# Optimization experiments

Hardware: AMD Instinct MI355X
Metric: run time of the kernel (lower is better)

## Reference

```python
import jax, jax.numpy as jnp
import numpy as np
from jax import lax

B, C, N, T, K = 16, 64, 512, 64, 3
EPS = 1e-5


def _bn(x, g, b):
    # training-mode BatchNorm2d over (B, H=N, W=T) per channel
    m = jnp.mean(x, axis=(0, 2, 3), keepdims=True)
    v = jnp.var(x, axis=(0, 2, 3), keepdims=True)
    return (x - m) * lax.rsqrt(v + EPS) * g[None, :, None, None] + b[None, :, None, None]


def _conv(x, w, b, pad):
    y = lax.conv_general_dilated(x, w, (1, 1), ((0, 0), pad),
                                 dimension_numbers=('NCHW', 'OIHW', 'NCHW'))
    return y + b[None, :, None, None]


def setup_inputs() -> dict:
    key = jax.random.key(0)
    ks = jax.random.split(key, 8)
    xav = lambda k, sh, fi, fo: jax.random.normal(k, sh, jnp.float32) * np.sqrt(2.0 / (fi + fo))
    return {
        'x': jax.random.normal(ks[0], (B, C, N, T), jnp.float32),
        'adj_mx': jax.random.normal(ks[1], (K, N, N), jnp.float32) / np.sqrt(N),
        'cheb_w': xav(ks[2], (K, C, C), C, C),
        'cheb_b': jnp.zeros((C,), jnp.float32),
        'w1': xav(ks[3], (C, C, 1, 3), 3 * C, 3 * C),
        'b1': jnp.zeros((C,), jnp.float32),
        'g1': jnp.ones((C,), jnp.float32),
        'be1': jnp.zeros((C,), jnp.float32),
        'w2': xav(ks[4], (C, C, 1, 3), 3 * C, 3 * C),
        'b2': jnp.zeros((C,), jnp.float32),
        'g2': jnp.ones((C,), jnp.float32),
        'be2': jnp.zeros((C,), jnp.float32),
        'gate_w': xav(ks[5], (C, 2 * C, 1, 1), 2 * C, C),
        'gate_b': jnp.zeros((C,), jnp.float32),
        'res_w': xav(ks[6], (C, C, 1, 1), C, C),
        'res_b': jnp.zeros((C,), jnp.float32),
        'g3': jnp.ones((C,), jnp.float32),
        'be3': jnp.zeros((C,), jnp.float32),
    }


def _forward(x, adj_mx, cheb_w, cheb_b, w1, b1, g1, be1, w2, b2, g2, be2,
             gate_w, gate_b, res_w, res_b, g3, be3):
    # ChebFilterBlock: out[b,o,n,t] = sum_{k,i,m} x[b,i,m,t] adj[k,m,n] W[k,i,o] + bias
    spatial = jnp.einsum('bimt,kmn,kio->bont', x, adj_mx, cheb_w) \
              + cheb_b[None, :, None, None]
    # temporal branch: two (1,3) convs with BN+ReLU
    t = jax.nn.relu(_bn(_conv(x, w1, b1, (1, 1)), g1, be1))
    t = jax.nn.relu(_bn(_conv(t, w2, b2, (1, 1)), g2, be2))
    # gated fusion
    comb = jnp.concatenate([spatial, t], axis=1)
    gate = jax.nn.sigmoid(_conv(comb, gate_w, gate_b, (0, 0)))
    res = _conv(x, res_w, res_b, (0, 0))
    out = gate * spatial + (1.0 - gate) * t + res
    return _bn(out, g3, be3)


def reference(x, adj_mx, cheb_w, cheb_b, w1, b1, g1, be1, w2, b2, g2, be2,
              gate_w, gate_b, res_w, res_b, g3, be3):
    return _forward(x, adj_mx, cheb_w, cheb_b, w1, b1, g1, be1, w2, b2, g2, be2,
                    gate_w, gate_b, res_w, res_b, g3, be3)
```

## Files before the change

kernel.cpp:

```cpp
#include <hip/hip_runtime.h>
#include <hip/hip_bf16.h>
#include <cstdint>

#define BB 16
#define CC 64
#define NN 512
#define TT 64
#define KCH 3
#define PP (BB*NN*TT)
#define EPSB 1e-5f

typedef __bf16 bf16;
typedef __bf16 bf16x8 __attribute__((ext_vector_type(8)));
typedef __bf16 bf16x4 __attribute__((ext_vector_type(4)));
typedef float  f32x4  __attribute__((ext_vector_type(4)));

#define MFMA16(A,Bv,Cv) __builtin_amdgcn_mfma_f32_16x16x32_bf16((A),(Bv),(Cv),0,0,0)

__device__ __forceinline__ void gload_lds16(const bf16* g, bf16* l){
  __builtin_amdgcn_global_load_lds(
      (const __attribute__((address_space(1))) void*)g,
      (__attribute__((address_space(3))) void*)l, 16, 0, 0);
}

__global__ __launch_bounds__(256) void k_adjT(const float* __restrict__ adj,
                                              bf16* __restrict__ adjb){
  int idx = blockIdx.x*256 + threadIdx.x;
  int m = idx & 511, n = (idx >> 9) & 511, k = idx >> 18;
  adjb[idx] = (bf16)adj[((size_t)(k*512 + m))*512 + n];
}

__global__ __launch_bounds__(256) void k_wprep(const float* __restrict__ w1,
    const float* __restrict__ w2, const float* __restrict__ cw,
    const float* __restrict__ gw, const float* __restrict__ rw,
    bf16* __restrict__ w1p, bf16* __restrict__ w2p, bf16* __restrict__ cp,
    bf16* __restrict__ gp, bf16* __restrict__ rp){
  int tid = threadIdx.x;
  for (int e = tid; e < 6*2048; e += 256){
    int j = e&7, lane = (e>>3)&63, cf = (e>>9)&3, ks = e>>11;
    int k = ks*32 + (lane>>4)*8 + j, col = cf*16 + (lane&15);
    int kk = k >> 6, i = k & 63;
    w1p[e] = (bf16)w1[(col*64 + i)*3 + kk];
    w2p[e] = (bf16)w2[(col*64 + i)*3 + kk];
    cp[e]  = (bf16)cw[((size_t)kk*64 + i)*64 + col];
  }
  for (int e = tid; e < 4*2048; e += 256){
    int j = e&7, lane = (e>>3)&63, cf = (e>>9)&3, ks = e>>11;
    int k = ks*32 + (lane>>4)*8 + j, col = cf*16 + (lane&15);
    gp[e] = (bf16)gw[col*128 + k];
  }
  for (int e = tid; e < 2*2048; e += 256){
    int j = e&7, lane = (e>>3)&63, cf = (e>>9)&3, ks = e>>11;
    int k = ks*32 + (lane>>4)*8 + j, col = cf*16 + (lane&15);
    rp[e] = (bf16)rw[col*64 + k];
  }
}

__global__ __launch_bounds__(256) void k_xlb(const float* __restrict__ x,
                                             bf16* __restrict__ xlb){
  __shared__ float tile[64][65];
  int bn = blockIdx.x; int b = bn >> 9, n = bn & 511;
  int tid = threadIdx.x;
  const float* xp = x + ((size_t)(b*64)*512 + n)*64;
  for (int p = 0; p < 4; ++p){
    int q = p*256 + tid;
    int i = q >> 4, tc = (q & 15)*4;
    float4 v = *reinterpret_cast<const float4*>(xp + (size_t)i*512*64 + tc);
    tile[i][tc+0] = v.x; tile[i][tc+1] = v.y; tile[i][tc+2] = v.z; tile[i][tc+3] = v.w;
  }
  __syncthreads();
  bf16* op = xlb + (size_t)bn*4096;
  for (int p = 0; p < 2; ++p){
    int v8 = p*256 + tid;
    int t = v8 >> 3, ic = (v8 & 7)*8;
    bf16x8 o;
    #pragma unroll
    for (int e = 0; e < 8; ++e) o[e] = (bf16)tile[ic+e][t];
    *reinterpret_cast<bf16x8*>(op + t*64 + ic) = o;
  }
}

__global__ __launch_bounds__(256) void k_xmt(const float* __restrict__ x,
                                             bf16* __restrict__ xmt){
  __shared__ bf16 lds[16][16][72];
  int bid = blockIdx.x;
  int t0 = (bid & 3)*16, m0 = ((bid>>2)&7)*64, i0 = ((bid>>5)&3)*16, b = bid>>7;
  int tid = threadIdx.x;
  int tq = tid & 3, m = tid >> 2;
  for (int i = 0; i < 16; ++i){
    float4 v = *reinterpret_cast<const float4*>(
        x + ((size_t)(b*64 + i0 + i)*512 + (m0 + m))*64 + t0 + tq*4);
    lds[tq*4+0][i][m] = (bf16)v.x; lds[tq*4+1][i][m] = (bf16)v.y;
    lds[tq*4+2][i][m] = (bf16)v.z; lds[tq*4+3][i][m] = (bf16)v.w;
  }
  __syncthreads();
  for (int p = 0; p < 8; ++p){
    int row = p*32 + (tid >> 3); int t = row >> 4, i = row & 15, mc = tid & 7;
    bf16x8 v = *reinterpret_cast<const bf16x8*>(&lds[t][i][mc*8]);
    *reinterpret_cast<bf16x8*>(
        xmt + ((size_t)((b*64 + t0 + t)*64) + i0 + i)*512 + m0 + mc*8) = v;
  }
}

__global__ __launch_bounds__(256,4) void k_conv(const bf16* __restrict__ in,
    const bf16* __restrict__ wp, bf16* __restrict__ outp, float* __restrict__ part,
    const float* __restrict__ sc, const float* __restrict__ sh){
  int tid = threadIdx.x, w = tid >> 6, l = tid & 63, l15 = l & 15, lg = l >> 4;
  int blk = blockIdx.x;
  size_t rowbase = (size_t)blk * 64;
  const bf16* xr = in + rowbase * 64;
  int t = w*16 + l15;
  f32x4 acc[4] = {};
  #pragma unroll
  for (int ks = 0; ks < 6; ++ks){
    int dt = ks >> 1, kh = ks & 1;
    int ts = t + dt - 1;
    bf16x8 a = {};
    if (ts >= 0 && ts < 64){
      a = *reinterpret_cast<const bf16x8*>(xr + ts*64 + kh*32 + lg*8);
      if (sc){
        int i0 = kh*32 + lg*8;
        #pragma unroll
        for (int e = 0; e < 8; ++e){
          float f = (float)a[e]*sc[i0+e] + sh[i0+e];
          a[e] = (bf16)fmaxf(f, 0.f);
        }
      }
    }
    #pragma unroll
    for (int cf = 0; cf < 4; ++cf){
      bf16x8 bfr = *reinterpret_cast<const bf16x8*>(wp + ((ks*4 + cf)*64 + l)*8);
      acc[cf] = MFMA16(a, bfr, acc[cf]);
    }
  }
  __shared__ float ssum[4][4][16], ssq[4][4][16];
  #pragma unroll
  for (int cf = 0; cf < 4; ++cf){
    int o = cf*16 + l15;
    float s = 0.f, q = 0.f;
    #pragma unroll
    for (int r = 0; r < 4; ++r){
      float vv = acc[cf][r];
      int to = w*16 + lg*4 + r;
      outp[(rowbase + to)*64 + o] = (bf16)vv;
      s += vv; q += vv*vv;
    }
    s += __shfl_xor(s, 16); s += __shfl_xor(s, 32);
    q += __shfl_xor(q, 16); q += __shfl_xor(q, 32);
    if (lg == 0){ ssum[w][cf][l15] = s; ssq[w][cf][l15] = q; }
  }
  __syncthreads();
  if (tid < 64){
    int cf = tid >> 4, c = tid & 15;
    float s = ssum[0][cf][c]+ssum[1][cf][c]+ssum[2][cf][c]+ssum[3][cf][c];
    float q = ssq[0][cf][c]+ssq[1][cf][c]+ssq[2][cf][c]+ssq[3][cf][c];
    part[(size_t)blk*128 + tid*2]     = s;
    part[(size_t)blk*128 + tid*2 + 1] = q;
  }
}

__global__ __launch_bounds__(256) void k_stats(const float* __restrict__ part, int nb,
    const float* __restrict__ g, const float* __restrict__ be,
    float* __restrict__ sc, float* __restrict__ sh){
  int c = blockIdx.x, tid = threadIdx.x;
  float s = 0.f, q = 0.f;
  for (int i = tid; i < nb; i += 256){
    s += part[(size_t)i*128 + c*2];
    q += part[(size_t)i*128 + c*2 + 1];
  }
  __shared__ float rs[256], rq[256];
  rs[tid] = s; rq[tid] = q; __syncthreads();
  for (int st = 128; st > 0; st >>= 1){
    if (tid < st){ rs[tid] += rs[tid+st]; rq[tid] += rq[tid+st]; }
    __syncthreads();
  }
  if (tid == 0){
    float cnt = (float)PP;
    float mean = rs[0]/cnt, var = rq[0]/cnt - mean*mean;
    float r = rsqrtf(var + EPSB);
    sc[c] = g[c]*r;
    sh[c] = be[c] - mean*g[c]*r;
  }
}

__global__ __launch_bounds__(256,2) void k_gemm1(const bf16* __restrict__ xmt,
    const bf16* __restrict__ adjb, const bf16* __restrict__ cp,
    const float* __restrict__ cb, bf16* __restrict__ spm){
  __shared__ bf16 As[3][4096];
  __shared__ bf16 Bs[3][4096];
  __shared__ bf16 VT[128*128];

  int tid = threadIdx.x, w = tid >> 6, l = tid & 63, l15 = l & 15, lg = l >> 4;
  int wr = w >> 1, wc = w & 1;

  int orig = blockIdx.x;
  int wg = (orig & 7) * 256 + (orig >> 3);
  int jt = wg >> 2, nt = wg & 3;
  int J0 = jt*128, N0 = nt*128;

  const bf16* aglob = xmt + (size_t)J0*512;
  const bf16* bbase = adjb + (size_t)N0*512;

  auto stage = [&](int t){
    int buf = t % 3;
    const bf16* bg = bbase + (size_t)(t >> 4)*512*512;
    int m0 = (t & 15)*32;
    #pragma unroll
    for (int p = 0; p < 2; ++p){
      int q = p*256 + tid;
      int r = q & 127, c = q >> 7;
      gload_lds16(aglob + (size_t)r*512 + m0 + c*8, &As[buf][q*8]);
      gload_lds16(bg    + (size_t)r*512 + m0 + c*8, &Bs[buf][q*8]);
    }
  };

  f32x4 acc2[4][4] = {};
  f32x4 acc[4][4] = {};
  int tw = w >> 1;

  stage(0);
  for (int t = 0; t < 48; ++t){
    if (t < 47){
      stage(t+1);
      asm volatile("s_waitcnt vmcnt(4)" ::: "memory");
    } else {
      asm volatile("s_waitcnt vmcnt(0)" ::: "memory");
    }
    __builtin_amdgcn_s_barrier();
    __builtin_amdgcn_sched_barrier(0);

    int buf = t % 3;
    bf16x8 a[4], bb[4];
    #pragma unroll
    for (int rf = 0; rf < 4; ++rf){
      int row = wr*64 + rf*16 + l15;
      a[rf] = *reinterpret_cast<const bf16x8*>(&As[buf][(lg*128 + row)*8]);
    }
    #pragma unroll
    for (int cf = 0; cf < 4; ++cf){
      int row = wc*64 + cf*16 + l15;
      bb[cf] = *reinterpret_cast<const bf16x8*>(&Bs[buf][(lg*128 + row)*8]);
    }
    #pragma unroll
    for (int rf = 0; rf < 4; ++rf)
      #pragma unroll
      for (int cf = 0; cf < 4; ++cf)
        acc[rf][cf] = MFMA16(a[rf], bb[cf], acc[rf][cf]);

    if ((t & 15) == 15){
      int kk = t >> 4;
      #pragma unroll
      for (int rf = 0; rf < 4; ++rf){
        int jb = wr*8 + rf*2 + (lg >> 1);
        #pragma unroll
        for (int cf = 0; cf < 4; ++cf){
          int n = wc*64 + cf*16 + l15;
          bf16x4 pk;
          #pragma unroll
          for (int r = 0; r < 4; ++r) pk[r] = (bf16)acc[rf][cf][r];
          *reinterpret_cast<bf16x4*>(
              &VT[n*128 + ((jb ^ (n & 15)) << 3) + ((lg & 1) << 2)]) = pk;
          acc[rf][cf] = (f32x4){0.f, 0.f, 0.f, 0.f};
        }
      }
      asm volatile("s_waitcnt lgkmcnt(0)" ::: "memory");
      __builtin_amdgcn_sched_barrier(0);
      __builtin_amdgcn_s_barrier();

      #pragma unroll
      for (int ks2 = 0; ks2 < 2; ++ks2){
        bf16x8 bc[4];
        #pragma unroll
        for (int cf = 0; cf < 4; ++cf)
          bc[cf] = *reinterpret_cast<const bf16x8*>(
              cp + (((kk*2 + ks2)*4 + cf)*64 + l)*8);
        #pragma unroll
        for (int rf = 0; rf < 4; ++rf){
          int n = (w & 1)*64 + rf*16 + l15;
          int jb = tw*8 + ks2*4 + lg;
          bf16x8 a2 = *reinterpret_cast<const bf16x8*>(
              &VT[n*128 + ((jb ^ (n & 15)) << 3)]);
          #pragma unroll
          for (int cf = 0; cf < 4; ++cf)
            acc2[rf][cf] = MFMA16(a2, bc[cf], acc2[rf][cf]);
        }
      }
      asm volatile("s_waitcnt lgkmcnt(0)" ::: "memory");
      __builtin_amdgcn_sched_barrier(0);
      __builtin_amdgcn_s_barrier();
    }
  }

  bf16* SP = VT;
  float cbv[4];
  #pragma unroll
  for (int cf = 0; cf < 4; ++cf) cbv[cf] = cb[cf*16 + l15];
  #pragma unroll
  for (int rf = 0; rf < 4; ++rf){
    int rowb = w*64 + rf*16 + lg*4;
    #pragma unroll
    for (int cf = 0; cf < 4; ++cf){
      int o = cf*16 + l15;
      #pragma unroll
      for (int r = 0; r < 4; ++r)
        SP[(rowb + r)*64 + o] = (bf16)(acc2[rf][cf][r] + cbv[cf]);
    }
  }
  __syncthreads();
  int b = jt >> 5, t0 = (jt & 31)*2;
  #pragma unroll
  for (int q = 0; q < 8; ++q){
    int flat = q*256 + tid;
    int row = flat >> 3, oc = (flat & 7)*8;
    int tl = row >> 7, n = N0 + (row & 127);
    bf16x8 vv = *reinterpret_cast<const bf16x8*>(&SP[row*64 + oc]);
    *reinterpret_cast<bf16x8*>(
        &spm[(((size_t)b*512 + n)*64 + (t0 + tl))*64 + oc]) = vv;
  }
}

__global__ __launch_bounds__(256,4) void k_fusion(const bf16* __restrict__ spm,
    const bf16* __restrict__ t2, const bf16* __restrict__ xlb,
    const bf16* __restrict__ gp, const bf16* __restrict__ rp,
    const float* __restrict__ sc2, const float* __restrict__ sh2,
    const float* __restrict__ gateb, bf16* __restrict__ pre,
    float* __restrict__ part){
  int tid = threadIdx.x, w = tid >> 6, l = tid & 63, l15 = l & 15, lg = l >> 4;
  int blk = blockIdx.x;
  int b = blk >> 9, n = blk & 511;
  size_t rowbase = (size_t)blk * 64;
  int t = w*16 + l15;
  f32x4 ag[4] = {}, ar[4] = {};
  #pragma unroll
  for (int ks = 0; ks < 4; ++ks){
    bf16x8 a;
    if (ks < 2){
      a = *reinterpret_cast<const bf16x8*>(spm + (rowbase + t)*64 + ks*32 + lg*8);
    } else {
      int i0 = (ks-2)*32 + lg*8;
      bf16x8 raw = *reinterpret_cast<const bf16x8*>(t2 + (rowbase + t)*64 + i0);
      #pragma unroll
      for (int e = 0; e < 8; ++e){
        float f = (float)raw[e]*sc2[i0+e] + sh2[i0+e];
        a[e] = (bf16)fmaxf(f, 0.f);
      }
    }
    #pragma unroll
    for (int cf = 0; cf < 4; ++cf){
      bf16x8 bfr = *reinterpret_cast<const bf16x8*>(gp + ((ks*4 + cf)*64 + l)*8);
      ag[cf] = MFMA16(a, bfr, ag[cf]);
    }
  }
  #pragma unroll
  for (int ks = 0; ks < 2; ++ks){
    bf16x8 a = *reinterpret_cast<const bf16x8*>(xlb + (rowbase + t)*64 + ks*32 + lg*8);
    #pragma unroll
    for (int cf = 0; cf < 4; ++cf){
      bf16x8 bfr = *reinterpret_cast<const bf16x8*>(rp + ((ks*4 + cf)*64 + l)*8);
      ar[cf] = MFMA16(a, bfr, ar[cf]);
    }
  }
  __shared__ float ssum[4][4][16], ssq[4][4][16];
  int tb = w*16 + lg*4;
  #pragma unroll
  for (int cf = 0; cf < 4; ++cf){
    int o = cf*16 + l15;
    float gb = gateb[o], sco = sc2[o], sho = sh2[o];
    float s = 0.f, q = 0.f;
    bf16x4 ov;
    #pragma unroll
    for (int r = 0; r < 4; ++r){
      size_t row = rowbase + tb + r;
      float z = ag[cf][r] + gb;
      float g = 1.f/(1.f + __expf(-z));
      float spv = (float)spm[row*64 + o];
      float tv  = (float)t2[row*64 + o];
      tv = fmaxf(tv*sco + sho, 0.f);
      float val = g*spv + (1.f - g)*tv + ar[cf][r];
      ov[r] = (bf16)val;
      s += val; q += val*val;
    }
    *reinterpret_cast<bf16x4*>(pre + (((size_t)b*64 + o)*512 + n)*64 + tb) = ov;
    s += __shfl_xor(s, 16); s += __shfl_xor(s, 32);
    q += __shfl_xor(q, 16); q += __shfl_xor(q, 32);
    if (lg == 0){ ssum[w][cf][l15] = s; ssq[w][cf][l15] = q; }
  }
  __syncthreads();
  if (tid < 64){
    int cf = tid >> 4, c = tid & 15;
    float s = ssum[0][cf][c]+ssum[1][cf][c]+ssum[2][cf][c]+ssum[3][cf][c];
    float q = ssq[0][cf][c]+ssq[1][cf][c]+ssq[2][cf][c]+ssq[3][cf][c];
    part[(size_t)blk*128 + tid*2]     = s;
    part[(size_t)blk*128 + tid*2 + 1] = q;
  }
}

__global__ __launch_bounds__(256) void k_bn3(const bf16* __restrict__ pre,
    float* __restrict__ out,
    const float* __restrict__ sc, const float* __restrict__ sh){
  size_t total8 = (size_t)BB*CC*NN*TT/8;
  for (size_t i8 = (size_t)blockIdx.x*256 + threadIdx.x; i8 < total8;
       i8 += (size_t)gridDim.x*256){
    bf16x8 v = reinterpret_cast<const bf16x8*>(pre)[i8];
    int o = (int)(i8 >> 12) & 63;
    float a = sc[o], bsh = sh[o];
    float4 r0, r1;
    r0.x = (float)v[0]*a + bsh; r0.y = (float)v[1]*a + bsh;
    r0.z = (float)v[2]*a + bsh; r0.w = (float)v[3]*a + bsh;
    r1.x = (float)v[4]*a + bsh; r1.y = (float)v[5]*a + bsh;
    r1.z = (float)v[6]*a + bsh; r1.w = (float)v[7]*a + bsh;
    reinterpret_cast<float4*>(out)[i8*2]     = r0;
    reinterpret_cast<float4*>(out)[i8*2 + 1] = r1;
  }
}

extern "C" void kernel_launch(void* const* d_in, const int* in_sizes, int n_in,
                              void* d_out, int out_size, void* d_ws, size_t ws_size,
                              hipStream_t stream){
  (void)in_sizes; (void)n_in; (void)out_size; (void)ws_size;
  const float* x   = (const float*)d_in[0];
  const float* adj = (const float*)d_in[1];
  const float* cw  = (const float*)d_in[2];
  const float* cb  = (const float*)d_in[3];
  const float* w1  = (const float*)d_in[4];
  const float* g1  = (const float*)d_in[6];
  const float* be1 = (const float*)d_in[7];
  const float* w2  = (const float*)d_in[8];
  const float* g2  = (const float*)d_in[10];
  const float* be2 = (const float*)d_in[11];
  const float* gw  = (const float*)d_in[12];
  const float* gb  = (const float*)d_in[13];
  const float* rw  = (const float*)d_in[14];
  const float* g3  = (const float*)d_in[16];
  const float* be3 = (const float*)d_in[17];
  float* out = (float*)d_out;

  char* ws = (char*)d_ws;
  size_t off = 0;
  auto alloc = [&](size_t bytes)->char*{
    char* p = ws + off; off += (bytes + 255) & ~(size_t)255; return p;
  };
  bf16* xlb  = (bf16*)alloc((size_t)PP*64*2);
  bf16* xmt  = (bf16*)alloc((size_t)PP*64*2);
  bf16* t1   = (bf16*)alloc((size_t)PP*64*2);
  bf16* t2   = (bf16*)alloc((size_t)PP*64*2);
  bf16* spm  = t1;
  bf16* pre  = xmt;
  bf16* adjb = (bf16*)alloc((size_t)KCH*512*512*2);
  bf16* w1p  = (bf16*)alloc(6*2048*2);
  bf16* w2p  = (bf16*)alloc(6*2048*2);
  bf16* cp   = (bf16*)alloc(6*2048*2);
  bf16* gp   = (bf16*)alloc(4*2048*2);
  bf16* rp   = (bf16*)alloc(2*2048*2);
  float* part = (float*)alloc((size_t)8192*128*4);
  float* s1sc = (float*)alloc(256); float* s1sh = (float*)alloc(256);
  float* s2sc = (float*)alloc(256); float* s2sh = (float*)alloc(256);
  float* s3sc = (float*)alloc(256); float* s3sh = (float*)alloc(256);

  k_adjT <<<dim3(3072), dim3(256), 0, stream>>>(adj, adjb);
  k_wprep<<<dim3(1),    dim3(256), 0, stream>>>(w1, w2, cw, gw, rw, w1p, w2p, cp, gp, rp);
  k_xlb  <<<dim3(8192), dim3(256), 0, stream>>>(x, xlb);
  k_xmt  <<<dim3(2048), dim3(256), 0, stream>>>(x, xmt);

  k_conv <<<dim3(8192), dim3(256), 0, stream>>>(xlb, w1p, t1, part, nullptr, nullptr);
  k_stats<<<dim3(64),   dim3(256), 0, stream>>>(part, 8192, g1, be1, s1sc, s1sh);
  k_conv <<<dim3(8192), dim3(256), 0, stream>>>(t1, w2p, t2, part, s1sc, s1sh);
  k_stats<<<dim3(64),   dim3(256), 0, stream>>>(part, 8192, g2, be2, s2sc, s2sh);

  k_gemm1<<<dim3(2048), dim3(256), 0, stream>>>(xmt, adjb, cp, cb, spm);

  k_fusion<<<dim3(8192), dim3(256), 0, stream>>>(spm, t2, xlb, gp, rp,
                                                 s2sc, s2sh, gb, pre, part);
  k_stats<<<dim3(64),   dim3(256), 0, stream>>>(part, 8192, g3, be3, s3sc, s3sh);
  k_bn3  <<<dim3(2048), dim3(256), 0, stream>>>(pre, out, s3sc, s3sh);
}
```

Before: 674.8 us.

## Shrink gemm1 LDS footprint for higher occupancy and rework xmt transpose tiling

The fused adjacency GEMM kernel drops from triple to double buffering, halves the VT staging buffer by splitting the second (Chebyshev weight) GEMM and the epilogue into two halves, and swizzles the LDS tile layout for A/B. Together these cut LDS use so three workgroups fit per CU instead of two. The cost is an extra barrier every k-step and more barriers in the epilogue, plus a shallower prefetch pipeline. The x-to-xmt transpose kernel is also retiled to larger blocks (half the grid) with an XOR-swizzled LDS layout to reduce bank conflicts.

```diff
diff --git a/kernel.cpp b/kernel.cpp
--- a/kernel.cpp
+++ b/kernel.cpp
@@ -82,23 +82,35 @@
 
 __global__ __launch_bounds__(256) void k_xmt(const float* __restrict__ x,
                                              bf16* __restrict__ xmt){
-  __shared__ bf16 lds[16][16][72];
+  __shared__ bf16 T[32768];
   int bid = blockIdx.x;
-  int t0 = (bid & 3)*16, m0 = ((bid>>2)&7)*64, i0 = ((bid>>5)&3)*16, b = bid>>7;
+  int b = bid >> 6, i0 = ((bid >> 3) & 7)*8, m0 = (bid & 7)*64;
   int tid = threadIdx.x;
-  int tq = tid & 3, m = tid >> 2;
-  for (int i = 0; i < 16; ++i){
+  #pragma unroll 4
+  for (int it = 0; it < 32; ++it){
+    int flat = it*256 + tid;
+    int t4 = flat & 15, m = (flat >> 4) & 63, i = flat >> 10;
     float4 v = *reinterpret_cast<const float4*>(
-        x + ((size_t)(b*64 + i0 + i)*512 + (m0 + m))*64 + t0 + tq*4);
-    lds[tq*4+0][i][m] = (bf16)v.x; lds[tq*4+1][i][m] = (bf16)v.y;
-    lds[tq*4+2][i][m] = (bf16)v.z; lds[tq*4+3][i][m] = (bf16)v.w;
+        x + ((size_t)((b*64 + i0 + i)*512) + (m0 + m))*64 + t4*4);
+    int im = i*64 + m;
+    int slot = t4 ^ ((m ^ i) & 15);
+    bf16x4 pk; pk[0] = (bf16)v.x; pk[1] = (bf16)v.y; pk[2] = (bf16)v.z; pk[3] = (bf16)v.w;
+    *reinterpret_cast<bf16x4*>(&T[im*64 + slot*4]) = pk;
   }
   __syncthreads();
-  for (int p = 0; p < 8; ++p){
-    int row = p*32 + (tid >> 3); int t = row >> 4, i = row & 15, mc = tid & 7;
-    bf16x8 v = *reinterpret_cast<const bf16x8*>(&lds[t][i][mc*8]);
+  #pragma unroll 4
+  for (int it = 0; it < 16; ++it){
+    int flat = it*256 + tid;
+    int mc = flat & 7, i = (flat >> 3) & 7, t = flat >> 6;
+    bf16x8 o;
+    #pragma unroll
+    for (int e = 0; e < 8; ++e){
+      int m = mc*8 + e;
+      int slot = (t >> 2) ^ ((m ^ i) & 15);
+      o[e] = T[(i*64 + m)*64 + slot*4 + (t & 3)];
+    }
     *reinterpret_cast<bf16x8*>(
-        xmt + ((size_t)((b*64 + t0 + t)*64) + i0 + i)*512 + m0 + mc*8) = v;
+        &xmt[((size_t)((b*64 + t)*64) + i0 + i)*512 + m0 + mc*8]) = o;
   }
 }
 
@@ -183,12 +195,12 @@
   }
 }
 
-__global__ __launch_bounds__(256,2) void k_gemm1(const bf16* __restrict__ xmt,
+__global__ __launch_bounds__(256,3) void k_gemm1(const bf16* __restrict__ xmt,
     const bf16* __restrict__ adjb, const bf16* __restrict__ cp,
     const float* __restrict__ cb, bf16* __restrict__ spm){
-  __shared__ bf16 As[3][4096];
-  __shared__ bf16 Bs[3][4096];
-  __shared__ bf16 VT[128*128];
+  __shared__ bf16 As[2][4096];
+  __shared__ bf16 Bs[2][4096];
+  __shared__ bf16 VT[64*128];
 
   int tid = threadIdx.x, w = tid >> 6, l = tid & 63, l15 = l & 15, lg = l >> 4;
   int wr = w >> 1, wc = w & 1;
@@ -202,21 +214,23 @@
   const bf16* bbase = adjb + (size_t)N0*512;
 
   auto stage = [&](int t){
-    int buf = t % 3;
+    int buf = t & 1;
     const bf16* bg = bbase + (size_t)(t >> 4)*512*512;
     int m0 = (t & 15)*32;
     #pragma unroll
     for (int p = 0; p < 2; ++p){
-      int q = p*256 + tid;
-      int r = q & 127, c = q >> 7;
-      gload_lds16(aglob + (size_t)r*512 + m0 + c*8, &As[buf][q*8]);
-      gload_lds16(bg    + (size_t)r*512 + m0 + c*8, &Bs[buf][q*8]);
+      int idx = p*256 + tid;
+      int r = idx >> 2, c = idx & 3;
+      int cg = c ^ (r & 3);
+      gload_lds16(aglob + (size_t)r*512 + m0 + cg*8,
+                  &As[buf][(p*256 + w*64)*8]);
+      gload_lds16(bg + (size_t)r*512 + m0 + cg*8,
+                  &Bs[buf][(p*256 + w*64)*8]);
     }
   };
 
+  f32x4 acc[4][4] = {};
   f32x4 acc2[4][4] = {};
-  f32x4 acc[4][4] = {};
-  int tw = w >> 1;
 
   stage(0);
   for (int t = 0; t < 48; ++t){
@@ -229,17 +243,19 @@
     __builtin_amdgcn_s_barrier();
     __builtin_amdgcn_sched_barrier(0);
 
-    int buf = t % 3;
+    int buf = t & 1;
     bf16x8 a[4], bb[4];
     #pragma unroll
     for (int rf = 0; rf < 4; ++rf){
       int row = wr*64 + rf*16 + l15;
-      a[rf] = *reinterpret_cast<const bf16x8*>(&As[buf][(lg*128 + row)*8]);
+      a[rf] = *reinterpret_cast<const bf16x8*>(
+          &As[buf][row*32 + ((lg ^ (row & 3))*8)]);
     }
     #pragma unroll
     for (int cf = 0; cf < 4; ++cf){
       int row = wc*64 + cf*16 + l15;
-      bb[cf] = *reinterpret_cast<const bf16x8*>(&Bs[buf][(lg*128 + row)*8]);
+      bb[cf] = *reinterpret_cast<const bf16x8*>(
+          &Bs[buf][row*32 + ((lg ^ (row & 3))*8)]);
     }
     #pragma unroll
     for (int rf = 0; rf < 4; ++rf)
@@ -247,75 +263,94 @@
       for (int cf = 0; cf < 4; ++cf)
         acc[rf][cf] = MFMA16(a[rf], bb[cf], acc[rf][cf]);
 
+    asm volatile("s_waitcnt lgkmcnt(0)" ::: "memory");
+    __builtin_amdgcn_sched_barrier(0);
+    __builtin_amdgcn_s_barrier();
+
     if ((t & 15) == 15){
       int kk = t >> 4;
       #pragma unroll
-      for (int rf = 0; rf < 4; ++rf){
-        int jb = wr*8 + rf*2 + (lg >> 1);
+      for (int h = 0; h < 2; ++h){
+        if (wc == h){
+          #pragma unroll
+          for (int rf = 0; rf < 4; ++rf){
+            int jb = wr*8 + rf*2 + (lg >> 1);
+            #pragma unroll
+            for (int cf = 0; cf < 4; ++cf){
+              int nh = cf*16 + l15;
+              bf16x4 pk;
+              #pragma unroll
+              for (int r = 0; r < 4; ++r) pk[r] = (bf16)acc[rf][cf][r];
+              *reinterpret_cast<bf16x4*>(
+                  &VT[nh*128 + ((jb ^ (nh & 15)) << 3) + ((lg & 1) << 2)]) = pk;
+            }
+          }
+        }
+        asm volatile("s_waitcnt lgkmcnt(0)" ::: "memory");
+        __builtin_amdgcn_sched_barrier(0);
+        __builtin_amdgcn_s_barrier();
+
+        #pragma unroll
+        for (int ks2 = 0; ks2 < 2; ++ks2){
+          bf16x8 bc[4];
+          #pragma unroll
+          for (int cf = 0; cf < 4; ++cf)
+            bc[cf] = *reinterpret_cast<const bf16x8*>(
+                cp + (((kk*2 + ks2)*4 + cf)*64 + l)*8);
+          #pragma unroll
+          for (int rf2 = 0; rf2 < 2; ++rf2){
+            int nh = (w & 1)*32 + rf2*16 + l15;
+            int jb = (w >> 1)*8 + ks2*4 + lg;
+            bf16x8 a2 = *reinterpret_cast<const bf16x8*>(
+                &VT[nh*128 + ((jb ^ (nh & 15)) << 3)]);
+            #pragma unroll
+            for (int cf = 0; cf < 4; ++cf)
+              acc2[h*2 + rf2][cf] = MFMA16(a2, bc[cf], acc2[h*2 + rf2][cf]);
+          }
+        }
+        asm volatile("s_waitcnt lgkmcnt(0)" ::: "memory");
+        __builtin_amdgcn_sched_barrier(0);
+        __builtin_amdgcn_s_barrier();
+      }
+      #pragma unroll
+      for (int rf = 0; rf < 4; ++rf)
+        #pragma unroll
+        for (int cf = 0; cf < 4; ++cf)
+          acc[rf][cf] = (f32x4){0.f, 0.f, 0.f, 0.f};
+    }
+  }
+
+  bf16* SP = VT;
+  float cbv[4];
+  #pragma unroll
+  for (int cf = 0; cf < 4; ++cf) cbv[cf] = cb[cf*16 + l15];
+  int b = jt >> 5, t0 = (jt & 31)*2;
+  #pragma unroll
+  for (int hr = 0; hr < 2; ++hr){
+    if ((w >> 1) == hr){
+      #pragma unroll
+      for (int f = 0; f < 4; ++f){
+        int h = f >> 1, rf2 = f & 1;
+        int rowb = h*64 + (w & 1)*32 + rf2*16 + lg*4;
         #pragma unroll
         for (int cf = 0; cf < 4; ++cf){
-          int n = wc*64 + cf*16 + l15;
-          bf16x4 pk;
+          int o = cf*16 + l15;
           #pragma unroll
-          for (int r = 0; r < 4; ++r) pk[r] = (bf16)acc[rf][cf][r];
-          *reinterpret_cast<bf16x4*>(
-              &VT[n*128 + ((jb ^ (n & 15)) << 3) + ((lg & 1) << 2)]) = pk;
-          acc[rf][cf] = (f32x4){0.f, 0.f, 0.f, 0.f};
+          for (int r = 0; r < 4; ++r)
+            SP[(rowb + r)*64 + o] = (bf16)(acc2[f][cf][r] + cbv[cf]);
         }
       }
-      asm volatile("s_waitcnt lgkmcnt(0)" ::: "memory");
-      __builtin_amdgcn_sched_barrier(0);
-      __builtin_amdgcn_s_barrier();
-
-      #pragma unroll
-      for (int ks2 = 0; ks2 < 2; ++ks2){
-        bf16x8 bc[4];
-        #pragma unroll
-        for (int cf = 0; cf < 4; ++cf)
-          bc[cf] = *reinterpret_cast<const bf16x8*>(
-              cp + (((kk*2 + ks2)*4 + cf)*64 + l)*8);
-        #pragma unroll
-        for (int rf = 0; rf < 4; ++rf){
-          int n = (w & 1)*64 + rf*16 + l15;
-          int jb = tw*8 + ks2*4 + lg;
-          bf16x8 a2 = *reinterpret_cast<const bf16x8*>(
-              &VT[n*128 + ((jb ^ (n & 15)) << 3)]);
-          #pragma unroll
-          for (int cf = 0; cf < 4; ++cf)
-            acc2[rf][cf] = MFMA16(a2, bc[cf], acc2[rf][cf]);
-        }
-      }
-      asm volatile("s_waitcnt lgkmcnt(0)" ::: "memory");
-      __builtin_amdgcn_sched_barrier(0);
-      __builtin_amdgcn_s_barrier();
-    }
-  }
-
-  bf16* SP = VT;
-  float cbv[4];
-  #pragma unroll
-  for (int cf = 0; cf < 4; ++cf) cbv[cf] = cb[cf*16 + l15];
-  #pragma unroll
-  for (int rf = 0; rf < 4; ++rf){
-    int rowb = w*64 + rf*16 + lg*4;
-    #pragma unroll
-    for (int cf = 0; cf < 4; ++cf){
-      int o = cf*16 + l15;
-      #pragma unroll
-      for (int r = 0; r < 4; ++r)
-        SP[(rowb + r)*64 + o] = (bf16)(acc2[rf][cf][r] + cbv[cf]);
-    }
-  }
-  __syncthreads();
-  int b = jt >> 5, t0 = (jt & 31)*2;
-  #pragma unroll
-  for (int q = 0; q < 8; ++q){
-    int flat = q*256 + tid;
-    int row = flat >> 3, oc = (flat & 7)*8;
-    int tl = row >> 7, n = N0 + (row & 127);
-    bf16x8 vv = *reinterpret_cast<const bf16x8*>(&SP[row*64 + oc]);
-    *reinterpret_cast<bf16x8*>(
-        &spm[(((size_t)b*512 + n)*64 + (t0 + tl))*64 + oc]) = vv;
+    }
+    __syncthreads();
+    #pragma unroll
+    for (int q = 0; q < 4; ++q){
+      int flat = q*256 + tid;
+      int n = flat >> 3, oc = (flat & 7)*8;
+      bf16x8 vv = *reinterpret_cast<const bf16x8*>(&SP[n*64 + oc]);
+      *reinterpret_cast<bf16x8*>(
+          &spm[(((size_t)b*512 + N0 + n)*64 + (t0 + hr))*64 + oc]) = vv;
+    }
+    __syncthreads();
   }
 }
 
@@ -460,7 +495,7 @@
   k_adjT <<<dim3(3072), dim3(256), 0, stream>>>(adj, adjb);
   k_wprep<<<dim3(1),    dim3(256), 0, stream>>>(w1, w2, cw, gw, rw, w1p, w2p, cp, gp, rp);
   k_xlb  <<<dim3(8192), dim3(256), 0, stream>>>(x, xlb);
-  k_xmt  <<<dim3(2048), dim3(256), 0, stream>>>(x, xmt);
+  k_xmt  <<<dim3(1024), dim3(256), 0, stream>>>(x, xmt);
 
   k_conv <<<dim3(8192), dim3(256), 0, stream>>>(xlb, w1p, t1, part, nullptr, nullptr);
   k_stats<<<dim3(64),   dim3(256), 0, stream>>>(part, 8192, g1, be1, s1sc, s1sh);
```

New measurement: 656.2 us. 2.8% less time.
